# Performance work log

Hardware: AMD Instinct MI355X
Metric: run time of the kernel (lower is better)

The kernel has to match this reference:

```python
import jax, jax.numpy as jnp
import numpy as np

EPS = 1e-9

def _gumbel_softmax(logits, u):
    # torch: noise.add_(1e-9).log_().neg_() twice -> g = -log(-log(u+eps)+eps)
    g = -jnp.log(-jnp.log(u + EPS) + EPS)
    return jax.nn.softmax(logits + g, axis=-1)  # tau=1, temperature=0

def setup_inputs() -> dict:
    key = jax.random.key(0)
    ks = jax.random.split(key, 8)
    n_obs, n_topics, n_dim, batch = 8192, 128, 64, 8192
    return {
        "pij": jax.random.uniform(ks[0], (batch,), jnp.float32, 1e-6, 1.0),
        "noise_full": jax.random.uniform(ks[1], (n_obs, n_topics), jnp.float32),
        "noise_i": jax.random.uniform(ks[2], (batch, n_topics), jnp.float32),
        "noise_j": jax.random.uniform(ks[3], (batch, n_topics), jnp.float32),
        "logits_weight": jax.random.normal(ks[4], (n_obs, n_topics), jnp.float32),
        "topic_w": jax.random.normal(ks[5], (n_dim, n_topics), jnp.float32) * 0.1,
        "topic_b": jax.random.normal(ks[6], (n_dim,), jnp.float32) * 0.1,
        "i": jax.random.randint(ks[7], (batch,), 0, n_obs),
        "j": jax.random.randint(jax.random.fold_in(key, 7), (batch,), 0, n_obs),
    }

def reference(pij, noise_full, noise_i, noise_j, logits_weight, topic_w, topic_b, i, j):
    topic = lambda z: z @ topic_w.T + topic_b
    # x: [n_obs, n_dim]
    x = topic(_gumbel_softmax(logits_weight, noise_full))
    # pairwise squared distances via norm trick (same math as expand-sub-square-sum)
    sq = jnp.sum(x * x, axis=-1)                      # [n_obs]
    dkl2 = sq[:, None] + sq[None, :] - 2.0 * (x @ x.T)  # [n_obs, n_obs]
    n_diagonal = dkl2.shape[0]
    part = jnp.sum(1.0 / (1.0 + dkl2)) - n_diagonal
    xi = topic(_gumbel_softmax(logits_weight[i], noise_i))  # [B, n_dim]
    xj = topic(_gumbel_softmax(logits_weight[j], noise_j))
    # faithful to source: sum of (1 + diff^2) over dims, then reciprocal
    num = 1.0 / jnp.sum(1.0 + (xi - xj) ** 2, axis=1)
    qij = num / part
    loss_kld = pij * (jnp.log(pij) - jnp.log(qij))
    return loss_kld
```

## Files before the change

### kernel.cpp

```cpp
#include <hip/hip_runtime.h>
#include <hip/hip_bf16.h>


typedef short bf16x8 __attribute__((ext_vector_type(8)));
typedef float f32x4 __attribute__((ext_vector_type(4)));

__device__ __forceinline__ float wave_sum(float v) {
#pragma unroll
  for (int off = 32; off; off >>= 1) v += __shfl_xor(v, off);
  return v;
}

__device__ __forceinline__ unsigned short f2bf(float x) {
  union { float f; unsigned u; } v; v.f = x;
  return (unsigned short)((v.u + 0x7fffu + ((v.u >> 16) & 1u)) >> 16);
}
__device__ __forceinline__ float bf2f(unsigned short h) {
  union { float f; unsigned u; } v; v.u = ((unsigned)h) << 16;
  return v.f;
}

__device__ __forceinline__ void gumbel_mfma(const float* __restrict__ lgp,
                                            const float* __restrict__ nzp,
                                            const bf16x8 Bf[4][4], f32x4 acc[4]) {
  float e[32];
  float ps = 0.0f;
#pragma unroll
  for (int ks = 0; ks < 4; ++ks) {
#pragma unroll
    for (int h = 0; h < 2; ++h) {
      float4 L = *(const float4*)(lgp + ks * 32 + h * 4);
      float4 U = *(const float4*)(nzp + ks * 32 + h * 4);
      float lv[4] = {L.x, L.y, L.z, L.w};
      float uv[4] = {U.x, U.y, U.z, U.w};
#pragma unroll
      for (int j = 0; j < 4; ++j) {
        float g = -__logf(-__logf(uv[j] + 1e-9f) + 1e-9f);
        float ev = __expf(lv[j] + g);
        e[ks * 8 + h * 4 + j] = ev;
        ps += ev;
      }
    }
  }
  ps += __shfl_xor(ps, 16);
  ps += __shfl_xor(ps, 32);
  float inv = __builtin_amdgcn_rcpf(ps);
#pragma unroll
  for (int ks = 0; ks < 4; ++ks) {
    union { bf16x8 v; unsigned short s[8]; } pk;
#pragma unroll
    for (int j = 0; j < 8; ++j) pk.s[j] = f2bf(e[ks * 8 + j] * inv);
#pragma unroll
    for (int nt = 0; nt < 4; ++nt)
      acc[nt] = __builtin_amdgcn_mfma_f32_16x16x32_bf16(pk.v, Bf[nt][ks], acc[nt], 0, 0, 0);
  }
}

__global__ __launch_bounds__(256) void row_engine(
    const float* __restrict__ logits, const float* __restrict__ noise_f,
    const float* __restrict__ noise_i, const float* __restrict__ noise_j,
    const float* __restrict__ topic_w, const float* __restrict__ tb,
    const int* __restrict__ ii, const int* __restrict__ jj,
    unsigned short* __restrict__ xb, float* __restrict__ sq,
    float* __restrict__ denomS) {
  int w = threadIdx.x >> 6, lane = threadIdx.x & 63;
  int r = lane & 15, part = lane >> 4;
  int wid = blockIdx.x * 4 + w;

  bf16x8 Bf[4][4];
#pragma unroll
  for (int nt = 0; nt < 4; ++nt) {
    const float* wp = topic_w + (nt * 16 + r) * 128 + part * 8;
#pragma unroll
    for (int ks = 0; ks < 4; ++ks) {
      float4 w0 = *(const float4*)(wp + ks * 32);
      float4 w1 = *(const float4*)(wp + ks * 32 + 4);
      union { bf16x8 v; unsigned short s[8]; } pk;
      pk.s[0] = f2bf(w0.x); pk.s[1] = f2bf(w0.y); pk.s[2] = f2bf(w0.z); pk.s[3] = f2bf(w0.w);
      pk.s[4] = f2bf(w1.x); pk.s[5] = f2bf(w1.y); pk.s[6] = f2bf(w1.z); pk.s[7] = f2bf(w1.w);
      Bf[nt][ks] = pk.v;
    }
  }
  int grp = wid >> 1;
  if ((wid & 1) == 0) {
    int g16 = grp * 16;
    float tbv[4];
#pragma unroll
    for (int nt = 0; nt < 4; ++nt) tbv[nt] = tb[nt * 16 + r];
    f32x4 acc[4] = {};
    gumbel_mfma(logits + (g16 + r) * 128 + part * 8,
                noise_f + (g16 + r) * 128 + part * 8, Bf, acc);
    float sqp[4] = {0.f, 0.f, 0.f, 0.f};
#pragma unroll
    for (int nt = 0; nt < 4; ++nt)
#pragma unroll
      for (int g = 0; g < 4; ++g) {
        unsigned short hb = f2bf(acc[nt][g] + tbv[nt]);
        xb[(g16 + part * 4 + g) * 64 + nt * 16 + r] = hb;
        float xr = bf2f(hb);
        sqp[g] += xr * xr;
      }
#pragma unroll
    for (int m = 1; m < 16; m <<= 1)
#pragma unroll
      for (int g = 0; g < 4; ++g) sqp[g] += __shfl_xor(sqp[g], m);
    if (r == 0) {
#pragma unroll
      for (int g = 0; g < 4; ++g) sq[g16 + part * 4 + g] = sqp[g];
    }
  } else {
    int b0 = grp * 16;
    int rowi = ii[b0 + r], rowj = jj[b0 + r];
    f32x4 ai[4] = {}, aj[4] = {};
    gumbel_mfma(logits + rowi * 128 + part * 8,
                noise_i + (b0 + r) * 128 + part * 8, Bf, ai);
    gumbel_mfma(logits + rowj * 128 + part * 8,
                noise_j + (b0 + r) * 128 + part * 8, Bf, aj);
    float dp[4] = {0.f, 0.f, 0.f, 0.f};
#pragma unroll
    for (int nt = 0; nt < 4; ++nt)
#pragma unroll
      for (int g = 0; g < 4; ++g) {
        float d = ai[nt][g] - aj[nt][g];
        dp[g] += d * d;
      }
#pragma unroll
    for (int m = 1; m < 16; m <<= 1)
#pragma unroll
      for (int g = 0; g < 4; ++g) dp[g] += __shfl_xor(dp[g], m);
    if (r == 0) {
#pragma unroll
      for (int g = 0; g < 4; ++g) denomS[b0 + part * 4 + g] = 64.0f + dp[g];
    }
  }
}

__global__ __launch_bounds__(256) void pairwise(const unsigned short* __restrict__ xbp,
                                                const float* __restrict__ sq,
                                                float* __restrict__ partial) {
  int w = threadIdx.x >> 6, lane = threadIdx.x & 63;
  int t = blockIdx.x, bi = 0;
  while (t >= 64 - bi) { t -= 64 - bi; ++bi; }
  int bj = bi + t;
  int wr = w >> 1, wc = w & 1;
  bool diag = (bi == bj);
  float local = 0.0f;
  if (!(diag && wr > wc)) {
    int R = bi * 128 + wr * 64;
    int C = bj * 128 + wc * 64;
    int r0 = lane & 15, kq = lane >> 4;

    bf16x8 A[4][2], B[4][2];
#pragma unroll
    for (int a = 0; a < 4; ++a)
#pragma unroll
      for (int s = 0; s < 2; ++s) {
        A[a][s] = *(const bf16x8*)(xbp + (R + a * 16 + r0) * 64 + s * 32 + kq * 8);
        B[a][s] = *(const bf16x8*)(xbp + (C + a * 16 + r0) * 64 + s * 32 + kq * 8);
      }
    f32x4 acc[4][4] = {};
#pragma unroll
    for (int a = 0; a < 4; ++a)
#pragma unroll
      for (int b = 0; b < 4; ++b) {
        acc[a][b] = __builtin_amdgcn_mfma_f32_16x16x32_bf16(A[a][0], B[b][0], acc[a][b], 0, 0, 0);
        acc[a][b] = __builtin_amdgcn_mfma_f32_16x16x32_bf16(A[a][1], B[b][1], acc[a][b], 0, 0, 0);
      }
    float m1[4][4], nsq[4];
#pragma unroll
    for (int a = 0; a < 4; ++a)
#pragma unroll
      for (int g = 0; g < 4; ++g) m1[a][g] = 1.0f + sq[R + a * 16 + kq * 4 + g];
#pragma unroll
    for (int b = 0; b < 4; ++b) nsq[b] = sq[C + b * 16 + r0];

    if (diag && wr == wc) {
#pragma unroll
      for (int a = 0; a < 4; ++a)
#pragma unroll
        for (int b = 0; b < 4; ++b)
#pragma unroll
          for (int g = 0; g < 4; ++g) {
            float d = fmaf(-2.0f, acc[a][b][g], m1[a][g] + nsq[b]);
            int rl = a * 16 + kq * 4 + g, cl = b * 16 + r0;
            local += (rl < cl) ? __builtin_amdgcn_rcpf(d) : 0.0f;
          }
    } else {
#pragma unroll
      for (int a = 0; a < 4; ++a)
#pragma unroll
        for (int b = 0; b < 4; ++b)
#pragma unroll
          for (int g = 0; g < 4; ++g) {
            float d = fmaf(-2.0f, acc[a][b][g], m1[a][g] + nsq[b]);
            local += __builtin_amdgcn_rcpf(d);
          }
    }
  }
  local = wave_sum(local);
  if (lane == 0) partial[blockIdx.x * 4 + w] = local;
}

__global__ __launch_bounds__(256) void finalize(const float* __restrict__ pij,
                                                const float* __restrict__ denomS,
                                                const float* __restrict__ partial,
                                                float* __restrict__ out) {
  __shared__ float red[4];
  int tid = threadIdx.x, w = tid >> 6, lane = tid & 63;
  float ps = 0.0f;
  for (int k = tid; k < 2080 * 4; k += 256) ps += partial[k];
  ps = wave_sum(ps);
  if (lane == 0) red[w] = ps;
  __syncthreads();
  float part = 2.0f * (red[0] + red[1] + red[2] + red[3]);
  int b = blockIdx.x * 256 + tid;
  float p = pij[b];
  out[b] = p * (__logf(p) + __logf(denomS[b]) + __logf(part));
}

extern "C" void kernel_launch(void* const* d_in, const int* in_sizes, int n_in,
                              void* d_out, int out_size, void* d_ws, size_t ws_size,
                              hipStream_t stream) {
  const float* pij     = (const float*)d_in[0];
  const float* noise_f = (const float*)d_in[1];
  const float* noise_i = (const float*)d_in[2];
  const float* noise_j = (const float*)d_in[3];
  const float* logits  = (const float*)d_in[4];
  const float* topic_w = (const float*)d_in[5];
  const float* tb      = (const float*)d_in[6];
  const int*   ii      = (const int*)d_in[7];
  const int*   jj      = (const int*)d_in[8];
  float* out = (float*)d_out;

  char* ws = (char*)d_ws;
  float* partial     = (float*)ws;
  unsigned short* xb = (unsigned short*)(ws + 33280);
  float* sq          = (float*)(ws + 33280 + 1048576);
  float* denomS      = (float*)(ws + 33280 + 1048576 + 32768);

  row_engine<<<256, 256, 0, stream>>>(logits, noise_f, noise_i, noise_j,
                                      topic_w, tb, ii, jj, xb, sq, denomS);
  pairwise<<<2080, 256, 0, stream>>>(xb, sq, partial);
  finalize<<<32, 256, 0, stream>>>(pij, denomS, partial, out);
}
```

Baseline: 123.7 us.

## Process four column tiles per pairwise block, reusing row fragments

```diff
diff --git a/kernel.cpp b/kernel.cpp
--- a/kernel.cpp
+++ b/kernel.cpp
@@ -135,70 +135,84 @@
   }
 }
 
+#define NPAIR_BLOCKS 544
 __global__ __launch_bounds__(256) void pairwise(const unsigned short* __restrict__ xbp,
                                                 const float* __restrict__ sq,
                                                 float* __restrict__ partial) {
+  __shared__ float red[4];
   int w = threadIdx.x >> 6, lane = threadIdx.x & 63;
-  int t = blockIdx.x, bi = 0;
-  while (t >= 64 - bi) { t -= 64 - bi; ++bi; }
-  int bj = bi + t;
+  int b = blockIdx.x, bi = 0, nch = 16;
+  while (b >= nch) { b -= nch; ++bi; nch = (64 - bi + 3) >> 2; }
+  int cj0 = bi + (b << 2);
   int wr = w >> 1, wc = w & 1;
-  bool diag = (bi == bj);
+  int R = bi * 128 + wr * 64;
+  int r0 = lane & 15, kq = lane >> 4;
+
+  bf16x8 A[4][2];
+#pragma unroll
+  for (int a = 0; a < 4; ++a)
+#pragma unroll
+    for (int s = 0; s < 2; ++s)
+      A[a][s] = *(const bf16x8*)(xbp + (R + a * 16 + r0) * 64 + s * 32 + kq * 8);
+  float m1[4][4];
+#pragma unroll
+  for (int a = 0; a < 4; ++a)
+#pragma unroll
+    for (int g = 0; g < 4; ++g) m1[a][g] = 1.0f + sq[R + a * 16 + kq * 4 + g];
+
   float local = 0.0f;
-  if (!(diag && wr > wc)) {
-    int R = bi * 128 + wr * 64;
+  int bjEnd = min(cj0 + 4, 64);
+  for (int bj = cj0; bj < bjEnd; ++bj) {
+    bool diagT = (bj == bi);
+    if (diagT && wr > wc) continue;
     int C = bj * 128 + wc * 64;
-    int r0 = lane & 15, kq = lane >> 4;
-
-    bf16x8 A[4][2], B[4][2];
+
+    bf16x8 B[4][2];
 #pragma unroll
     for (int a = 0; a < 4; ++a)
 #pragma unroll
-      for (int s = 0; s < 2; ++s) {
-        A[a][s] = *(const bf16x8*)(xbp + (R + a * 16 + r0) * 64 + s * 32 + kq * 8);
+      for (int s = 0; s < 2; ++s)
         B[a][s] = *(const bf16x8*)(xbp + (C + a * 16 + r0) * 64 + s * 32 + kq * 8);
-      }
+    float nsq[4];
+#pragma unroll
+    for (int q = 0; q < 4; ++q) nsq[q] = sq[C + q * 16 + r0];
+
     f32x4 acc[4][4] = {};
 #pragma unroll
     for (int a = 0; a < 4; ++a)
 #pragma unroll
-      for (int b = 0; b < 4; ++b) {
-        acc[a][b] = __builtin_amdgcn_mfma_f32_16x16x32_bf16(A[a][0], B[b][0], acc[a][b], 0, 0, 0);
-        acc[a][b] = __builtin_amdgcn_mfma_f32_16x16x32_bf16(A[a][1], B[b][1], acc[a][b], 0, 0, 0);
-      }
-    float m1[4][4], nsq[4];
-#pragma unroll
-    for (int a = 0; a < 4; ++a)
-#pragma unroll
-      for (int g = 0; g < 4; ++g) m1[a][g] = 1.0f + sq[R + a * 16 + kq * 4 + g];
-#pragma unroll
-    for (int b = 0; b < 4; ++b) nsq[b] = sq[C + b * 16 + r0];
-
-    if (diag && wr == wc) {
+      for (int q = 0; q < 4; ++q) {
+        acc[a][q] = __builtin_amdgcn_mfma_f32_16x16x32_bf16(A[a][0], B[q][0], acc[a][q], 0, 0, 0);
+        acc[a][q] = __builtin_amdgcn_mfma_f32_16x16x32_bf16(A[a][1], B[q][1], acc[a][q], 0, 0, 0);
+      }
+
+    if (diagT && wr == wc) {
 #pragma unroll
       for (int a = 0; a < 4; ++a)
 #pragma unroll
-        for (int b = 0; b < 4; ++b)
+        for (int q = 0; q < 4; ++q)
 #pragma unroll
           for (int g = 0; g < 4; ++g) {
-            float d = fmaf(-2.0f, acc[a][b][g], m1[a][g] + nsq[b]);
-            int rl = a * 16 + kq * 4 + g, cl = b * 16 + r0;
+            float d = fmaf(-2.0f, acc[a][q][g], m1[a][g] + nsq[q]);
+            int rl = a * 16 + kq * 4 + g, cl = q * 16 + r0;
             local += (rl < cl) ? __builtin_amdgcn_rcpf(d) : 0.0f;
           }
     } else {
 #pragma unroll
       for (int a = 0; a < 4; ++a)
 #pragma unroll
-        for (int b = 0; b < 4; ++b)
+        for (int q = 0; q < 4; ++q)
 #pragma unroll
           for (int g = 0; g < 4; ++g) {
-            float d = fmaf(-2.0f, acc[a][b][g], m1[a][g] + nsq[b]);
+            float d = fmaf(-2.0f, acc[a][q][g], m1[a][g] + nsq[q]);
             local += __builtin_amdgcn_rcpf(d);
           }
     }
   }
   local = wave_sum(local);
-  if (lane == 0) partial[blockIdx.x * 4 + w] = local;
+  if (lane == 0) red[w] = local;
+  __syncthreads();
+  if (threadIdx.x == 0) partial[blockIdx.x] = red[0] + red[1] + red[2] + red[3];
 }
 
 __global__ __launch_bounds__(256) void finalize(const float* __restrict__ pij,
@@ -208,7 +222,7 @@
   __shared__ float red[4];
   int tid = threadIdx.x, w = tid >> 6, lane = tid & 63;
   float ps = 0.0f;
-  for (int k = tid; k < 2080 * 4; k += 256) ps += partial[k];
+  for (int k = tid; k < NPAIR_BLOCKS; k += 256) ps += partial[k];
   ps = wave_sum(ps);
   if (lane == 0) red[w] = ps;
   __syncthreads();
@@ -234,12 +248,12 @@
 
   char* ws = (char*)d_ws;
   float* partial     = (float*)ws;
-  unsigned short* xb = (unsigned short*)(ws + 33280);
-  float* sq          = (float*)(ws + 33280 + 1048576);
-  float* denomS      = (float*)(ws + 33280 + 1048576 + 32768);
+  unsigned short* xb = (unsigned short*)(ws + 8192);
+  float* sq          = (float*)(ws + 8192 + 1048576);
+  float* denomS      = (float*)(ws + 8192 + 1048576 + 32768);
 
   row_engine<<<256, 256, 0, stream>>>(logits, noise_f, noise_i, noise_j,
                                       topic_w, tb, ii, jj, xb, sq, denomS);
-  pairwise<<<2080, 256, 0, stream>>>(xb, sq, partial);
+  pairwise<<<NPAIR_BLOCKS, 256, 0, stream>>>(xb, sq, partial);
   finalize<<<32, 256, 0, stream>>>(pij, denomS, partial, out);
 }
```

Result: faster. 115.8 us (-6.4%).
